# Kernel tuning notes

Measured on AMD Instinct MI355X. Metric: run time of the kernel, lower is better.

Reference implementation:

```python
import jax, jax.numpy as jnp
import numpy as np
from jax import lax

B, C, H, W = 4, 32, 224, 224
KH, KW = 5, 5
KK = KH * KW
L = H * W


def setup_inputs() -> dict:
    key = jax.random.key(0)
    k1, k2, k3, k4 = jax.random.split(key, 4)
    return {
        "input_tensor": jax.random.normal(k1, (B, C, H, W), dtype=jnp.float32),
        "color_distance_tensor": jax.random.uniform(k2, (B, L, KK), dtype=jnp.float32),
        "color_weight": jax.random.uniform(k3, (1,), dtype=jnp.float32, minval=-0.005, maxval=0.005),
        "position_weight": jax.random.uniform(k4, (1,), dtype=jnp.float32, minval=-0.005, maxval=0.005),
    }


def reference(input_tensor, color_distance_tensor, color_weight, position_weight):
    kh, kw = KH, KW
    # torch F.pad(pad=(a,b,c,d)) pads LAST dim (width) with (a,b) and 2nd-last (height) with (c,d).
    # The source passes (kh//2,(kh-1)//2, kw//2,(kw-1)//2) -> width padded by kh-based, height by kw-based.
    pw_l, pw_r = kh // 2, (kh - 1) // 2
    ph_t, ph_b = kw // 2, (kw - 1) // 2
    padded = jnp.pad(input_tensor, ((0, 0), (0, 0), (ph_t, ph_b), (pw_l, pw_r)))
    # im2col: features ordered (C, kh, kw) like torch.nn.Unfold -> (B, C*KK, H, W)
    patches = lax.conv_general_dilated_patches(padded, (kh, kw), (1, 1), "VALID")
    unf = patches.reshape(B, C * KK, L).transpose(0, 2, 1)  # (B, L, C*KK)
    # replicate torch's reshape of the non-contiguous permuted tensor (index scramble):
    unf = unf.reshape(B, C, KK, L).transpose(0, 1, 3, 2)  # (B, C, L, KK)
    # position distances: (height_pos - kh//2)^2 (1,kh) + (width_pos - kw//2)^2 transposed (kw,1)
    hd = (jnp.arange(kh) - kh // 2) ** 2
    wd = (jnp.arange(kw) - kw // 2) ** 2
    pos = (hd[None, :] + wd[:, None]).reshape(-1).astype(jnp.float32)  # (KK,)
    weights = pos * position_weight + color_distance_tensor * color_weight  # (B, L, KK)
    weights = weights[:, None]  # (B, 1, L, KK) == torch unsqueeze(dim=1)
    out = (unf * weights).sum(-1).reshape(B, C, H, W)
    return out * input_tensor
```

## Files before the change

kernel.cpp:

```cpp
#include <hip/hip_runtime.h>

#define BB 4
#define CC 32
#define LL 50176
#define KK2 25
#define CDTOT (BB * LL * KK2)


typedef const float __attribute__((address_space(1)))* gcd_ptr;
typedef float __attribute__((address_space(3)))* lds_ptr;

__global__ __launch_bounds__(256) void conv_local_kernel(
    const float* __restrict__ input,
    const float* __restrict__ cd,
    const float* __restrict__ colw,
    const float* __restrict__ posw,
    float* __restrict__ out)
{
    __shared__ float smem[6656];

    const int t    = threadIdx.x;
    const int lane = t & 63;
    const int w    = t >> 6;

    const int bx   = blockIdx.x;
    const int xcd  = bx & 7;
    const int slot = bx >> 3;
    const int b    = xcd >> 1;
    const int j    = slot * 2 + (xcd & 1);
    const int chunk  = j & 1;
    const int rem0   = (j >> 1) * 4;
    const int c2base = chunk * 16;

    const float cw = colw[0];
    const float pw = posw[0];
    const float* __restrict__ in_b  = input + b * (CC * LL);
    float* __restrict__       out_b = out   + b * (CC * LL);

    {
        const int cd_base = b * (LL * KK2);
        #pragma unroll
        for (int jj = 0; jj < 26; ++jj) {
            int s    = t + 256 * jj;
            int ci   = s / 101;
            int pos  = s - ci * 101;
            int gidx = cd_base + (rem0 + 800 * ci) * KK2 + pos;
            gidx = min(gidx, CDTOT - 1);
            __builtin_amdgcn_global_load_lds((gcd_ptr)(cd + gidx),
                                             (lds_ptr)(smem + (jj * 256 + w * 64)),
                                             4, 0, 0);
        }
    }
    __syncthreads();

    const int remU = __builtin_amdgcn_readfirstlane(rem0 + w);
    const int ii   = lane;

    float Wt[KK2];
    int   A0u[KK2];
    const float POS[KK2] = {8,5,4,5,8, 5,2,1,2,5, 4,1,0,1,4, 5,2,1,2,5, 8,5,4,5,8};

    #pragma unroll
    for (int k2 = 0; k2 < KK2; ++k2) {
        int t1 = 576 * k2 + remU;
        int q0 = t1 / 800;
        int r  = t1 - q0 * 800;
        int c  = r / 25;
        int s  = r - c * 25;
        int dy = s / 5 - 2;
        int dx = s % 5 - 2;
        int e0 = 62 * k2 + q0;
        A0u[k2] = c * LL + 224 * dy + dx + e0;
        int u  = e0 + ii;
        int ys = u / 224;
        int xs = u - ys * 224;
        int xm = xs + dx;
        bool xok = (unsigned)xm < 224u;
        float wgt = fmaf(smem[ii * 101 + w * 25 + k2], cw, POS[k2] * pw);
        Wt[k2] = xok ? wgt : 0.0f;
    }
    __syncthreads();

    const int remB = t & 3;
    const int iiB  = t >> 2;
    const int l2B  = rem0 + remB + 800 * iiB;
    const bool okB = l2B < LL;
    const int idxB = min(l2B, LL - 1);

    #pragma unroll 1
    for (int gg = 0; gg < 2; ++gg) {
        float acc[8], iv[8];
        #pragma unroll
        for (int g = 0; g < 8; ++g) {
            acc[g] = 0.0f;
            iv[g]  = in_b[(c2base + gg * 8 + g) * LL + idxB];
        }

        #pragma unroll
        for (int k2 = 0; k2 < KK2; ++k2) {
            const float wv = Wt[k2];
            #pragma unroll
            for (int g = 0; g < 8; ++g) {
                int c2  = c2base + gg * 8 + g;
                int c2e = min(max(c2, 1), 30);
                const float* bp = in_b + (A0u[k2] + 1568 * c2e);
                acc[g] = fmaf(bp[ii], wv, acc[g]);
            }
        }

        const bool sp_here = (chunk == 0) ? (gg == 0) : (gg == 1);
        if (sp_here) {
            const bool sp0 = (chunk == 0);
            float a = 0.0f;
            #pragma unroll
            for (int k2 = 0; k2 < KK2; ++k2) {
                int t1 = 576 * k2 + remU;
                int q0 = t1 / 800;
                int r  = t1 - q0 * 800;
                int c  = r / 25;
                int s  = r - c * 25;
                int dy = s / 5 - 2;
                int dx = s % 5 - 2;
                int u  = 62 * k2 + q0 + ii;
                int ys = u / 224;
                int xs = u - ys * 224;
                int xc = min(max(xs + dx, 0), 223);
                int yy = ys + dy;
                int yb = sp0 ? max(yy, 0) : (217 + min(yy, 6));
                bool ok = sp0 ? (yy >= 0) : (yy <= 6);
                float v = in_b[c * LL + yb * 224 + xc];
                a = fmaf(ok ? v : 0.0f, Wt[k2], a);
            }
            if (sp0) acc[0] = a; else acc[7] = a;
        }

        float* sbuf = smem + gg * 2560;
        #pragma unroll
        for (int g = 0; g < 8; ++g)
            sbuf[g * 320 + w * 80 + lane] = acc[g];
        __syncthreads();
        #pragma unroll
        for (int g = 0; g < 8; ++g) {
            float S = sbuf[g * 320 + remB * 80 + iiB];
            if (okB) out_b[(c2base + gg * 8 + g) * LL + idxB] = S * iv[g];
        }
    }
}

extern "C" void kernel_launch(void* const* d_in, const int* in_sizes, int n_in,
                              void* d_out, int out_size, void* d_ws, size_t ws_size,
                              hipStream_t stream) {
    const float* input = (const float*)d_in[0];
    const float* cdist = (const float*)d_in[1];
    const float* cwp   = (const float*)d_in[2];
    const float* pwp   = (const float*)d_in[3];
    float* o = (float*)d_out;

    dim3 grid(1600);
    dim3 block(256);
    hipLaunchKernelGGL(conv_local_kernel, grid, block, 0, stream,
                       input, cdist, cwp, pwp, o);
}
```

Baseline: 138.9 us.

## Vectorize gather loads to float2 with weights staged in LDS

```diff
diff --git a/kernel.cpp b/kernel.cpp
--- a/kernel.cpp
+++ b/kernel.cpp
@@ -10,6 +10,8 @@
 typedef const float __attribute__((address_space(1)))* gcd_ptr;
 typedef float __attribute__((address_space(3)))* lds_ptr;
 
+#define WOFF 6656
+
 __global__ __launch_bounds__(256) void conv_local_kernel(
     const float* __restrict__ input,
     const float* __restrict__ cd,
@@ -17,7 +19,7 @@
     const float* __restrict__ posw,
     float* __restrict__ out)
 {
-    __shared__ float smem[6656];
+    __shared__ float smem[13056];
 
     const int t    = threadIdx.x;
     const int lane = t & 63;
@@ -56,8 +58,7 @@
     const int remU = __builtin_amdgcn_readfirstlane(rem0 + w);
     const int ii   = lane;
 
-    float Wt[KK2];
-    int   A0u[KK2];
+    int A0u[KK2];
     const float POS[KK2] = {8,5,4,5,8, 5,2,1,2,5, 4,1,0,1,4, 5,2,1,2,5, 8,5,4,5,8};
 
     #pragma unroll
@@ -77,7 +78,7 @@
         int xm = xs + dx;
         bool xok = (unsigned)xm < 224u;
         float wgt = fmaf(smem[ii * 101 + w * 25 + k2], cw, POS[k2] * pw);
-        Wt[k2] = xok ? wgt : 0.0f;
+        smem[WOFF + w * 1600 + k2 * 64 + ii] = xok ? wgt : 0.0f;
     }
     __syncthreads();
 
@@ -87,25 +88,41 @@
     const bool okB = l2B < LL;
     const int idxB = min(l2B, LL - 1);
 
+    const int m  = lane & 31;
+    const int hi = lane >> 5;
+    const int voffN  = 1568 * hi + 2 * m;
+    const int voffLo = 1568 + 2 * m;
+    const int voffHi = 2 * m;
+
     #pragma unroll 1
     for (int gg = 0; gg < 2; ++gg) {
-        float acc[8], iv[8];
+        float acc0[4], acc1[4], iv[8];
         #pragma unroll
-        for (int g = 0; g < 8; ++g) {
-            acc[g] = 0.0f;
-            iv[g]  = in_b[(c2base + gg * 8 + g) * LL + idxB];
-        }
+        for (int gp = 0; gp < 4; ++gp) { acc0[gp] = 0.0f; acc1[gp] = 0.0f; }
+        #pragma unroll
+        for (int g = 0; g < 8; ++g)
+            iv[g] = in_b[(c2base + gg * 8 + g) * LL + idxB];
 
         #pragma unroll
         for (int k2 = 0; k2 < KK2; ++k2) {
-            const float wv = Wt[k2];
+            const float2 wp = *(const float2*)&smem[WOFF + w * 1600 + k2 * 64 + 2 * m];
             #pragma unroll
-            for (int g = 0; g < 8; ++g) {
-                int c2  = c2base + gg * 8 + g;
-                int c2e = min(max(c2, 1), 30);
-                const float* bp = in_b + (A0u[k2] + 1568 * c2e);
-                acc[g] = fmaf(bp[ii], wv, acc[g]);
+            for (int gp = 0; gp < 4; ++gp) {
+                const bool spLo = (chunk == 0) && (gg == 0) && (gp == 0);
+                const bool spHi = (chunk == 1) && (gg == 1) && (gp == 3);
+                const int offE = spLo ? voffLo : (spHi ? voffHi : voffN);
+                const float* bp = in_b + (A0u[k2] + 1568 * (c2base + gg * 8 + 2 * gp));
+                const float2 v = *(const float2*)(bp + offE);
+                acc0[gp] = fmaf(v.x, wp.x, acc0[gp]);
+                acc1[gp] = fmaf(v.y, wp.y, acc1[gp]);
             }
+        }
+
+        float* sbuf = smem + (gg & 1) * 2560;
+        #pragma unroll
+        for (int gp = 0; gp < 4; ++gp) {
+            const int gl = 2 * gp + hi;
+            *(float2*)&sbuf[gl * 320 + w * 80 + 2 * m] = make_float2(acc0[gp], acc1[gp]);
         }
 
         const bool sp_here = (chunk == 0) ? (gg == 0) : (gg == 1);
@@ -129,16 +146,13 @@
                 int yb = sp0 ? max(yy, 0) : (217 + min(yy, 6));
                 bool ok = sp0 ? (yy >= 0) : (yy <= 6);
                 float v = in_b[c * LL + yb * 224 + xc];
-                a = fmaf(ok ? v : 0.0f, Wt[k2], a);
+                float wk = smem[WOFF + w * 1600 + k2 * 64 + ii];
+                a = fmaf(ok ? v : 0.0f, wk, a);
             }
-            if (sp0) acc[0] = a; else acc[7] = a;
+            sbuf[(sp0 ? 0 : 7) * 320 + w * 80 + lane] = a;
         }
+        __syncthreads();
 
-        float* sbuf = smem + gg * 2560;
-        #pragma unroll
-        for (int g = 0; g < 8; ++g)
-            sbuf[g * 320 + w * 80 + lane] = acc[g];
-        __syncthreads();
         #pragma unroll
         for (int g = 0; g < 8; ++g) {
             float S = sbuf[g * 320 + remB * 80 + iiB];
```

After: 157.6 us. 13.5% more time.
